# Kernel tuning notes

Hardware: AMD Instinct MI355X
Metric: run time of the kernel (lower is better)

## Reference

```python
import jax, jax.numpy as jnp
import numpy as np

# TT factorization of a 4096 -> 4096 linear layer
IN_SHAPE = (8, 8, 8, 8)    # input_tt_shape, prod = 4096
OUT_SHAPE = (8, 8, 8, 8)   # output_tt_shape, prod = 4096
RANKS = (1, 16, 16, 16, 1) # tt_ranks, len = n_dim + 1
N_DIM = len(IN_SHAPE)
BATCH = 2048
OUT_SIZE = int(np.prod(OUT_SHAPE))
IN_SIZE = int(np.prod(IN_SHAPE))


def setup_inputs() -> dict:
    key = jax.random.key(0)
    ks = jax.random.split(key, N_DIM + 1)
    x = jax.random.normal(ks[0], (BATCH, IN_SIZE), dtype=jnp.float32)
    inp = {"x": x}
    for i in range(N_DIM):
        rows = RANKS[i] * OUT_SHAPE[i]
        cols = IN_SHAPE[i] * RANKS[i + 1]
        # xavier_uniform scale, matching torch init statistics
        limit = float(np.sqrt(6.0 / (rows + cols)))
        inp[f"core{i}"] = jax.random.uniform(
            ks[i + 1], (rows, cols), minval=-limit, maxval=limit, dtype=jnp.float32
        )
    inp["bias"] = jnp.zeros((OUT_SIZE,), dtype=jnp.float32)
    return inp


def reference(x, core0, core1, core2, core3, bias):
    cores = [core0, core1, core2, core3]
    res = x  # [B, prod(IN_SHAPE)]
    # Sequential TT-core contraction, last mode first (faithful to torch loop)
    for k in range(N_DIM - 1, -1, -1):
        res = res.reshape(-1, IN_SHAPE[k])                     # [.., n_k]
        res = res.T                                            # [n_k, ..]
        res = res.reshape(RANKS[k + 1] * IN_SHAPE[k], -1)      # [r_{k+1}*n_k, ..]
        res = cores[k] @ res                                   # [r_k*m_k, ..]
    res = res.reshape(OUT_SIZE, -1).T                          # [B, prod(OUT_SHAPE)]
    return res + bias
```

## Files before the change

### kernel.cpp

```cpp
#include <hip/hip_runtime.h>
#include <hip/hip_bf16.h>
#include <stdint.h>


typedef __bf16 bf16_t;
typedef __bf16 bf16x8 __attribute__((ext_vector_type(8)));
typedef __bf16 bf16x4 __attribute__((ext_vector_type(4)));
typedef float floatx4 __attribute__((ext_vector_type(4)));

#define BATCH_N 2048
#define KD 4096
#define ND 4096

__device__ static inline void load_lds16(const void* g, void* l) {
    __builtin_amdgcn_global_load_lds(
        (const __attribute__((address_space(1))) void*)g,
        (__attribute__((address_space(3))) void*)l, 16, 0, 0);
}

__global__ __launch_bounds__(256) void prep0(const float* __restrict__ x,
                                             const float* __restrict__ c0,
                                             const float* __restrict__ c1,
                                             const float* __restrict__ c2,
                                             const float* __restrict__ c3,
                                             bf16_t* __restrict__ xb,
                                             float* __restrict__ Pg,
                                             float* __restrict__ Tg) {
    const int t = threadIdx.x;
    const int b = blockIdx.x;

    if (b < 4096) {
        int g = b * 256 + t;
        const float4* xv = (const float4*)x;
        float4 a = xv[g * 2];
        float4 c = xv[g * 2 + 1];
        bf16x8 o;
        o[0] = (bf16_t)a.x; o[1] = (bf16_t)a.y; o[2] = (bf16_t)a.z; o[3] = (bf16_t)a.w;
        o[4] = (bf16_t)c.x; o[5] = (bf16_t)c.y; o[6] = (bf16_t)c.z; o[7] = (bf16_t)c.w;
        ((bf16x8*)xb)[g] = o;
        return;
    }

    __shared__ float s0[128];
    __shared__ float s1[2048];

    if (b < 4160) {
        const int n01 = b - 4096, n0 = n01 >> 3, n1 = n01 & 7;
        if (t < 128) s0[t] = c0[(t >> 4) * 128 + n0 * 16 + (t & 15)];
        for (int i = t; i < 2048; i += 256) {
            int r1 = i >> 7, m1 = (i >> 4) & 7, r2 = i & 15;
            s1[i] = c1[(r1 * 8 + m1) * 128 + n1 * 16 + r2];
        }
        __syncthreads();
#pragma unroll
        for (int j = 0; j < 4; ++j) {
            int o = j * 256 + t, m01 = o >> 4, r2 = o & 15;
            int m0 = m01 >> 3, m1 = m01 & 7;
            float s = 0.f;
#pragma unroll
            for (int r1 = 0; r1 < 16; ++r1)
                s += s0[m0 * 16 + r1] * s1[r1 * 128 + m1 * 16 + r2];
            Pg[n01 * 1024 + o] = s;
        }
        return;
    }

    {
        const int m23 = b - 4160, m2 = m23 >> 3, m3 = m23 & 7;
        if (t < 128) s0[t] = c3[((t >> 3) * 8 + m3) * 8 + (t & 7)];
        for (int i = t; i < 2048; i += 256) {
            int r2 = i >> 7, n2 = (i >> 4) & 7, r3 = i & 15;
            s1[i] = c2[(r2 * 8 + m2) * 128 + n2 * 16 + r3];
        }
        __syncthreads();
#pragma unroll
        for (int j = 0; j < 4; ++j) {
            int o = j * 256 + t, n23 = o >> 4, r2 = o & 15;
            int n2 = n23 >> 3, n3 = n23 & 7;
            float s = 0.f;
#pragma unroll
            for (int r3 = 0; r3 < 16; ++r3)
                s += s1[r2 * 128 + n2 * 16 + r3] * s0[r3 * 8 + n3];
            Tg[m23 * 1024 + o] = s;
        }
    }
}

__global__ __launch_bounds__(256) void build_w(const float* __restrict__ Pg,
                                               const float* __restrict__ Tg,
                                               bf16_t* __restrict__ W) {
    const int t = threadIdx.x;
    const int b = blockIdx.x;
    const int n01 = b & 63, q = b >> 6;
    const int cg = t & 15;
    const int mr = t >> 4;
    const float* Pb = Pg + n01 * 1024 + q * 256;

#pragma unroll 1
    for (int ms = 0; ms < 4; ++ms) {
        const int m23 = ms * 16 + mr;
        float Tr[4][16];
#pragma unroll
        for (int jj = 0; jj < 4; ++jj) {
            const float4* tp = (const float4*)(Tg + (m23 * 64 + cg * 4 + jj) * 16);
#pragma unroll
            for (int w = 0; w < 4; ++w) {
                float4 v = tp[w];
                Tr[jj][w * 4 + 0] = v.x;
                Tr[jj][w * 4 + 1] = v.y;
                Tr[jj][w * 4 + 2] = v.z;
                Tr[jj][w * 4 + 3] = v.w;
            }
        }
#pragma unroll 4
        for (int ml = 0; ml < 16; ++ml) {
            float a0 = 0.f, a1 = 0.f, a2 = 0.f, a3 = 0.f;
#pragma unroll
            for (int r2 = 0; r2 < 16; ++r2) {
                float p = Pb[ml * 16 + r2];
                a0 += p * Tr[0][r2];
                a1 += p * Tr[1][r2];
                a2 += p * Tr[2][r2];
                a3 += p * Tr[3][r2];
            }
            bf16x4 o;
            o[0] = (bf16_t)a0; o[1] = (bf16_t)a1; o[2] = (bf16_t)a2; o[3] = (bf16_t)a3;
            *(bf16x4*)(W + (size_t)((q * 16 + ml) * 64 + m23) * 4096 + n01 * 64 + cg * 4) = o;
        }
    }
}

__global__ __launch_bounds__(512, 2) void gemm_bt2(const bf16_t* __restrict__ A,
                                                   const bf16_t* __restrict__ B,
                                                   const float* __restrict__ bias,
                                                   float* __restrict__ C) {
    __shared__ bf16_t smem[3][24576];
    const int t = threadIdx.x;
    const int bid = blockIdx.x;
    const int xcd = bid & 7, idx = bid >> 3;
    const int bm = xcd * 2 + (idx & 1);
    const int bn = idx >> 1;
    const int lane = t & 63, wave = t >> 6;
    const int wm = wave >> 2, wn = wave & 3;

    const int srow = t >> 3;
    const int lc = (t & 7) ^ (srow & 7);
    const bf16_t* Ag = A + (size_t)(bm * 128 + srow) * KD + lc * 8;
    const bf16_t* Bg = B + (size_t)(bn * 256 + srow) * KD + lc * 8;
    const int woff = wave * 512;

    floatx4 acc[4][4];
    floatx4 zero = {0.f, 0.f, 0.f, 0.f};
#pragma unroll
    for (int i = 0; i < 4; ++i)
#pragma unroll
        for (int j = 0; j < 4; ++j) acc[i][j] = zero;

    const int fr = lane & 15;
    const int fc = lane >> 4;

#pragma unroll
    for (int kt = 0; kt < 2; ++kt) {
        bf16_t* bb = &smem[kt][0];
        const size_t ko = (size_t)kt * 64;
#pragma unroll
        for (int c = 0; c < 2; ++c)
            load_lds16(Ag + (size_t)c * 64 * KD + ko, bb + c * 4096 + woff);
#pragma unroll
        for (int c = 0; c < 4; ++c)
            load_lds16(Bg + (size_t)c * 64 * KD + ko, bb + 8192 + c * 4096 + woff);
    }
    asm volatile("s_waitcnt vmcnt(6)\n\ts_barrier" ::: "memory");

    int cur = 0;
#pragma unroll 1
    for (int kt = 0; kt < 64; ++kt) {
        if (kt < 62) {
            int nb = cur + 2; if (nb >= 3) nb -= 3;
            bf16_t* bb = &smem[nb][0];
            const size_t ko = (size_t)(kt + 2) * 64;
#pragma unroll
            for (int c = 0; c < 2; ++c)
                load_lds16(Ag + (size_t)c * 64 * KD + ko, bb + c * 4096 + woff);
#pragma unroll
            for (int c = 0; c < 4; ++c)
                load_lds16(Bg + (size_t)c * 64 * KD + ko, bb + 8192 + c * 4096 + woff);
        }

        const bf16_t* Ab = &smem[cur][0];
        const bf16_t* Bb = &smem[cur][8192];
#pragma unroll
        for (int kk = 0; kk < 2; ++kk) {
            const int pA = (fc + kk * 4) ^ (fr & 7);
            bf16x8 af[4], bf[4];
#pragma unroll
            for (int im = 0; im < 4; ++im)
                af[im] = *(const bf16x8*)(Ab + (wm * 64 + im * 16 + fr) * 64 + pA * 8);
#pragma unroll
            for (int in = 0; in < 4; ++in)
                bf[in] = *(const bf16x8*)(Bb + (wn * 64 + in * 16 + fr) * 64 + pA * 8);
            __builtin_amdgcn_s_setprio(1);
#pragma unroll
            for (int im = 0; im < 4; ++im)
#pragma unroll
                for (int in = 0; in < 4; ++in)
                    acc[im][in] = __builtin_amdgcn_mfma_f32_16x16x32_bf16(
                        af[im], bf[in], acc[im][in], 0, 0, 0);
            __builtin_amdgcn_s_setprio(0);
        }

        if (kt < 62) {
            asm volatile("s_waitcnt vmcnt(6) lgkmcnt(0)\n\ts_barrier" ::: "memory");
        } else if (kt == 62) {
            asm volatile("s_waitcnt vmcnt(0) lgkmcnt(0)\n\ts_barrier" ::: "memory");
        }
        cur = (cur == 2) ? 0 : cur + 1;
    }

    const int rl = lane >> 4, cl = lane & 15;
    const size_t rbase = (size_t)bm * 128 + wm * 64;
    const int cbase = bn * 256 + wn * 64;
#pragma unroll
    for (int im = 0; im < 4; ++im) {
#pragma unroll
        for (int in = 0; in < 4; ++in) {
            int col = cbase + in * 16 + cl;
            float bv = bias[col];
#pragma unroll
            for (int r = 0; r < 4; ++r) {
                size_t row = rbase + im * 16 + rl * 4 + r;
                C[row * ND + col] = acc[im][in][r] + bv;
            }
        }
    }
}

extern "C" void kernel_launch(void* const* d_in, const int* in_sizes, int n_in,
                              void* d_out, int out_size, void* d_ws, size_t ws_size,
                              hipStream_t stream) {
    const float* x  = (const float*)d_in[0];
    const float* c0 = (const float*)d_in[1];
    const float* c1 = (const float*)d_in[2];
    const float* c2 = (const float*)d_in[3];
    const float* c3 = (const float*)d_in[4];
    const float* bias = (const float*)d_in[5];
    float* out = (float*)d_out;

    char* ws = (char*)d_ws;
    bf16_t* Xb = (bf16_t*)ws;
    bf16_t* W  = (bf16_t*)(ws + (16u << 20));

    float* Pg = (float*)d_out;
    float* Tg = Pg + 64 * 1024;

    prep0<<<4224, 256, 0, stream>>>(x, c0, c1, c2, c3, Xb, Pg, Tg);
    build_w<<<256, 256, 0, stream>>>(Pg, Tg, W);
    gemm_bt2<<<256, 512, 0, stream>>>(Xb, W, bias, out);
}
```

Measured before the change: 171.4 us.

## Interleave global-to-LDS prefetch with MFMA phases in GEMM main loop

Splits each K-tile iteration into four phases, each loading a subset of A/B fragments from LDS and running 8 MFMAs, with the global-to-LDS prefetch for the tile two steps ahead spread across the first three phases. Extra s_barrier and sched_barrier calls are added so the waves move through the phases in lockstep. The aim is to spread memory issue across the MFMA work and lower register pressure by holding only two B fragments at a time. In exchange, each iteration now has many more barriers, which can cost more than the overlap gains.

```diff
diff --git a/kernel.cpp b/kernel.cpp
--- a/kernel.cpp
+++ b/kernel.cpp
@@ -158,6 +158,8 @@
 
     const int fr = lane & 15;
     const int fc = lane >> 4;
+    const int pA0 = fc ^ (fr & 7);
+    const int pA1 = (fc + 4) ^ (fr & 7);
 
 #pragma unroll
     for (int kt = 0; kt < 2; ++kt) {
@@ -175,39 +177,83 @@
     int cur = 0;
 #pragma unroll 1
     for (int kt = 0; kt < 64; ++kt) {
-        if (kt < 62) {
-            int nb = cur + 2; if (nb >= 3) nb -= 3;
-            bf16_t* bb = &smem[nb][0];
-            const size_t ko = (size_t)(kt + 2) * 64;
-#pragma unroll
-            for (int c = 0; c < 2; ++c)
-                load_lds16(Ag + (size_t)c * 64 * KD + ko, bb + c * 4096 + woff);
-#pragma unroll
-            for (int c = 0; c < 4; ++c)
-                load_lds16(Bg + (size_t)c * 64 * KD + ko, bb + 8192 + c * 4096 + woff);
-        }
-
+        int nb = cur + 2; if (nb >= 3) nb -= 3;
+        bf16_t* bb = &smem[nb][0];
+        const size_t ko = (size_t)(kt + 2) * 64;
         const bf16_t* Ab = &smem[cur][0];
         const bf16_t* Bb = &smem[cur][8192];
-#pragma unroll
-        for (int kk = 0; kk < 2; ++kk) {
-            const int pA = (fc + kk * 4) ^ (fr & 7);
-            bf16x8 af[4], bf[4];
-#pragma unroll
-            for (int im = 0; im < 4; ++im)
-                af[im] = *(const bf16x8*)(Ab + (wm * 64 + im * 16 + fr) * 64 + pA * 8);
-#pragma unroll
-            for (int in = 0; in < 4; ++in)
-                bf[in] = *(const bf16x8*)(Bb + (wn * 64 + in * 16 + fr) * 64 + pA * 8);
-            __builtin_amdgcn_s_setprio(1);
-#pragma unroll
-            for (int im = 0; im < 4; ++im)
-#pragma unroll
-                for (int in = 0; in < 4; ++in)
-                    acc[im][in] = __builtin_amdgcn_mfma_f32_16x16x32_bf16(
-                        af[im], bf[in], acc[im][in], 0, 0, 0);
-            __builtin_amdgcn_s_setprio(0);
-        }
+        const bool st = (kt < 62);
+
+        bf16x8 af[4], bf0, bf1;
+
+        if (st) {
+            load_lds16(Ag + ko, bb + woff);
+            load_lds16(Ag + (size_t)64 * KD + ko, bb + 4096 + woff);
+        }
+#pragma unroll
+        for (int im = 0; im < 4; ++im)
+            af[im] = *(const bf16x8*)(Ab + (wm * 64 + im * 16 + fr) * 64 + pA0 * 8);
+        bf0 = *(const bf16x8*)(Bb + (wn * 64 + 0 * 16 + fr) * 64 + pA0 * 8);
+        bf1 = *(const bf16x8*)(Bb + (wn * 64 + 1 * 16 + fr) * 64 + pA0 * 8);
+        asm volatile("s_barrier\n\ts_waitcnt lgkmcnt(0)" ::: "memory");
+        __builtin_amdgcn_s_setprio(1);
+#pragma unroll
+        for (int im = 0; im < 4; ++im) {
+            acc[im][0] = __builtin_amdgcn_mfma_f32_16x16x32_bf16(af[im], bf0, acc[im][0], 0, 0, 0);
+            acc[im][1] = __builtin_amdgcn_mfma_f32_16x16x32_bf16(af[im], bf1, acc[im][1], 0, 0, 0);
+        }
+        __builtin_amdgcn_s_setprio(0);
+        __builtin_amdgcn_sched_barrier(0);
+        asm volatile("s_barrier" ::: "memory");
+
+        if (st) {
+            load_lds16(Bg + ko, bb + 8192 + woff);
+            load_lds16(Bg + (size_t)64 * KD + ko, bb + 8192 + 4096 + woff);
+        }
+        bf0 = *(const bf16x8*)(Bb + (wn * 64 + 2 * 16 + fr) * 64 + pA0 * 8);
+        bf1 = *(const bf16x8*)(Bb + (wn * 64 + 3 * 16 + fr) * 64 + pA0 * 8);
+        asm volatile("s_barrier\n\ts_waitcnt lgkmcnt(0)" ::: "memory");
+        __builtin_amdgcn_s_setprio(1);
+#pragma unroll
+        for (int im = 0; im < 4; ++im) {
+            acc[im][2] = __builtin_amdgcn_mfma_f32_16x16x32_bf16(af[im], bf0, acc[im][2], 0, 0, 0);
+            acc[im][3] = __builtin_amdgcn_mfma_f32_16x16x32_bf16(af[im], bf1, acc[im][3], 0, 0, 0);
+        }
+        __builtin_amdgcn_s_setprio(0);
+        __builtin_amdgcn_sched_barrier(0);
+        asm volatile("s_barrier" ::: "memory");
+
+        if (st) {
+            load_lds16(Bg + (size_t)128 * KD + ko, bb + 8192 + 2 * 4096 + woff);
+            load_lds16(Bg + (size_t)192 * KD + ko, bb + 8192 + 3 * 4096 + woff);
+        }
+#pragma unroll
+        for (int im = 0; im < 4; ++im)
+            af[im] = *(const bf16x8*)(Ab + (wm * 64 + im * 16 + fr) * 64 + pA1 * 8);
+        bf0 = *(const bf16x8*)(Bb + (wn * 64 + 0 * 16 + fr) * 64 + pA1 * 8);
+        bf1 = *(const bf16x8*)(Bb + (wn * 64 + 1 * 16 + fr) * 64 + pA1 * 8);
+        asm volatile("s_barrier\n\ts_waitcnt lgkmcnt(0)" ::: "memory");
+        __builtin_amdgcn_s_setprio(1);
+#pragma unroll
+        for (int im = 0; im < 4; ++im) {
+            acc[im][0] = __builtin_amdgcn_mfma_f32_16x16x32_bf16(af[im], bf0, acc[im][0], 0, 0, 0);
+            acc[im][1] = __builtin_amdgcn_mfma_f32_16x16x32_bf16(af[im], bf1, acc[im][1], 0, 0, 0);
+        }
+        __builtin_amdgcn_s_setprio(0);
+        __builtin_amdgcn_sched_barrier(0);
+        asm volatile("s_barrier" ::: "memory");
+
+        bf0 = *(const bf16x8*)(Bb + (wn * 64 + 2 * 16 + fr) * 64 + pA1 * 8);
+        bf1 = *(const bf16x8*)(Bb + (wn * 64 + 3 * 16 + fr) * 64 + pA1 * 8);
+        asm volatile("s_barrier\n\ts_waitcnt lgkmcnt(0)" ::: "memory");
+        __builtin_amdgcn_s_setprio(1);
+#pragma unroll
+        for (int im = 0; im < 4; ++im) {
+            acc[im][2] = __builtin_amdgcn_mfma_f32_16x16x32_bf16(af[im], bf0, acc[im][2], 0, 0, 0);
+            acc[im][3] = __builtin_amdgcn_mfma_f32_16x16x32_bf16(af[im], bf1, acc[im][3], 0, 0, 0);
+        }
+        __builtin_amdgcn_s_setprio(0);
+        __builtin_amdgcn_sched_barrier(0);
 
         if (kt < 62) {
             asm volatile("s_waitcnt vmcnt(6) lgkmcnt(0)\n\ts_barrier" ::: "memory");
```

Measured after the change: 174.8 us. Within noise of the previous version (+2.0%).
